# Optimization experiments

Hardware: AMD Instinct MI355X
Metric: run time of the kernel (lower is better)

## Reference

```python
import jax, jax.numpy as jnp
import numpy as np

B, T, D = 2, 2048, 2048
H, DH = 16, 128
FG = 5461
EPS = 1e-5
ROPE_BASE = 10000.0


def rmsnorm(x, w):
    rms = jax.lax.rsqrt(jnp.mean(x * x, axis=-1, keepdims=True) + EPS)
    return x * rms * w


def rotate_half(x):
    x1 = x[..., ::2]
    x2 = x[..., 1::2]
    return jnp.stack((-x2, x1), axis=-1).reshape(x.shape)


def rope_tables(t_len, dh, dtype):
    inv_freq = 1.0 / (ROPE_BASE ** (np.arange(0, dh, 2, dtype=np.float32) / dh))
    t = np.arange(t_len, dtype=np.float32)
    freqs = np.outer(t, inv_freq)                 # [T, dh/2]
    emb = np.repeat(freqs, 2, axis=-1)            # repeat_interleave -> [T, dh]
    return jnp.asarray(np.cos(emb), dtype), jnp.asarray(np.sin(emb), dtype)


def setup_inputs() -> dict:
    key = jax.random.key(0)
    ks = jax.random.split(key, 8)
    s_attn = 1.0 / np.sqrt(D)
    s_gate = 1.0 / np.sqrt(D)
    s_proj = 1.0 / np.sqrt(FG)
    return {
        "x": jax.random.normal(ks[0], (B, T, D), jnp.float32),
        "norm1_w": jnp.ones((D,), jnp.float32),
        "norm2_w": jnp.ones((D,), jnp.float32),
        "c_attn_w": jax.random.normal(ks[1], (3 * D, D), jnp.float32) * s_attn,
        "c_proj_w": jax.random.normal(ks[2], (D, D), jnp.float32) * s_attn,
        "c_gate_w": jax.random.normal(ks[3], (FG, D), jnp.float32) * s_gate,
        "c_val_w": jax.random.normal(ks[4], (FG, D), jnp.float32) * s_gate,
        "c_mlp_proj_w": jax.random.normal(ks[5], (D, FG), jnp.float32) * s_proj,
    }


def block(x, norm1_w, norm2_w, c_attn_w, c_proj_w, c_gate_w, c_val_w, c_mlp_proj_w):
    # ---- attention branch (pre-norm) ----
    h = rmsnorm(x, norm1_w)
    qkv = h @ c_attn_w.T                                   # [B,T,3D]
    qkv = qkv.reshape(B, T, 3, H, DH).transpose(2, 0, 3, 1, 4)
    q, k, v = qkv[0], qkv[1], qkv[2]                       # [B,H,T,DH]
    cos, sin = rope_tables(T, DH, x.dtype)                 # [T,DH]
    q = q * cos + rotate_half(q) * sin
    k = k * cos + rotate_half(k) * sin
    att = jnp.einsum("bhqd,bhkd->bhqk", q, k) * (1.0 / np.sqrt(DH))
    causal = jnp.tril(jnp.ones((T, T), bool))
    att = jnp.where(causal, att, -jnp.inf)
    att = jax.nn.softmax(att, axis=-1)
    y = jnp.einsum("bhqk,bhkd->bhqd", att, v)              # [B,H,T,DH]
    y = y.transpose(0, 2, 1, 3).reshape(B, T, D)
    x = x + y @ c_proj_w.T
    # ---- MLP branch (pre-norm, SwiGLU) ----
    h = rmsnorm(x, norm2_w)
    gate = jax.nn.silu(h @ c_gate_w.T)                     # [B,T,FG]
    val = h @ c_val_w.T
    x = x + (gate * val) @ c_mlp_proj_w.T
    return x


def reference(x, norm1_w, norm2_w, c_attn_w, c_proj_w, c_gate_w, c_val_w, c_mlp_proj_w):
    return block(x, norm1_w, norm2_w, c_attn_w, c_proj_w, c_gate_w, c_val_w, c_mlp_proj_w)
```

## Files before the change

### kernel.cpp

```cpp
#include <hip/hip_runtime.h>
#include <hip/hip_bf16.h>
#include <stdint.h>

typedef __bf16 bf16_t;
typedef __bf16 bf16x8 __attribute__((ext_vector_type(8)));
typedef float  f32x4  __attribute__((ext_vector_type(4)));

#define DEV __device__ __forceinline__

constexpr int   Bn = 2, Tn = 2048, Dn = 2048, Hn = 16, DHn = 128;
constexpr int   BTn = Bn * Tn;
constexpr int   TD3 = 3 * Dn;
constexpr int   FGn = 5461, FGPn = 5504;
constexpr float EPSf   = 1e-5f;
constexpr float LOG2E  = 1.4426950408889634f;
constexpr float ASCALE = 0.08838834764831845f;
constexpr float LN1E4  = 9.210340371976184f;

DEV void gld16(void* lds, const void* g) {
  __builtin_amdgcn_global_load_lds(
      (__attribute__((address_space(1))) void*)(void*)g,
      (__attribute__((address_space(3))) void*)lds, 16, 0, 0);
}

DEV bf16x8 dsr128(const bf16_t* p) {
  bf16x8 r;
  asm volatile("ds_read_b128 %0, %1"
               : "=v"(r)
               : "v"((const __attribute__((address_space(3))) bf16_t*)p));
  return r;
}

__global__ __launch_bounds__(256)
void rmsnorm_k(const float* __restrict__ x, const float* __restrict__ w,
               bf16_t* __restrict__ out) {
  const int row = blockIdx.x;
  const int tid = threadIdx.x;
  const float* xr = x + (size_t)row * Dn;
  float4 a = ((const float4*)xr)[tid * 2];
  float4 b = ((const float4*)xr)[tid * 2 + 1];
  float ss = a.x*a.x + a.y*a.y + a.z*a.z + a.w*a.w
           + b.x*b.x + b.y*b.y + b.z*b.z + b.w*b.w;
#pragma unroll
  for (int off = 32; off > 0; off >>= 1) ss += __shfl_xor(ss, off, 64);
  __shared__ float red[4];
  if ((tid & 63) == 0) red[tid >> 6] = ss;
  __syncthreads();
  float tot = red[0] + red[1] + red[2] + red[3];
  float rms = rsqrtf(tot * (1.0f / Dn) + EPSf);
  float4 wa = ((const float4*)w)[tid * 2];
  float4 wb = ((const float4*)w)[tid * 2 + 1];
  bf16x8 o;
  o[0] = (bf16_t)(a.x * rms * wa.x); o[1] = (bf16_t)(a.y * rms * wa.y);
  o[2] = (bf16_t)(a.z * rms * wa.z); o[3] = (bf16_t)(a.w * rms * wa.w);
  o[4] = (bf16_t)(b.x * rms * wb.x); o[5] = (bf16_t)(b.y * rms * wb.y);
  o[6] = (bf16_t)(b.z * rms * wb.z); o[7] = (bf16_t)(b.w * rms * wb.w);
  *(bf16x8*)&out[(size_t)row * Dn + tid * 8] = o;
}

__global__ __launch_bounds__(256)
void cvt_pad_k(const float* __restrict__ src, bf16_t* __restrict__ dst,
               int srcR, int srcC, int dstC, int n8) {
  int i = blockIdx.x * 256 + threadIdx.x;
  if (i >= n8) return;
  long base = (long)i * 8;
  int r = (int)(base / dstC);
  int c = (int)(base % dstC);
  bf16x8 o;
#pragma unroll
  for (int k = 0; k < 8; ++k) {
    int cc = c + k;
    float v = (r < srcR && cc < srcC) ? src[(size_t)r * srcC + cc] : 0.0f;
    o[k] = (bf16_t)v;
  }
  *(bf16x8*)&dst[base] = o;
}

__global__ __launch_bounds__(256)
void reduce_k(float* __restrict__ out, const bf16_t* __restrict__ P0,
              const bf16_t* __restrict__ P1) {
  int i = blockIdx.x * 256 + threadIdx.x;
  bf16x8 p0 = *(const bf16x8*)&P0[(size_t)i * 8];
  bf16x8 p1 = *(const bf16x8*)&P1[(size_t)i * 8];
  float4 o0 = ((const float4*)out)[i * 2];
  float4 o1 = ((const float4*)out)[i * 2 + 1];
  o0.x += (float)p0[0] + (float)p1[0];
  o0.y += (float)p0[1] + (float)p1[1];
  o0.z += (float)p0[2] + (float)p1[2];
  o0.w += (float)p0[3] + (float)p1[3];
  o1.x += (float)p0[4] + (float)p1[4];
  o1.y += (float)p0[5] + (float)p1[5];
  o1.z += (float)p0[6] + (float)p1[6];
  o1.w += (float)p0[7] + (float)p1[7];
  ((float4*)out)[i * 2]     = o0;
  ((float4*)out)[i * 2 + 1] = o1;
}

__global__ __launch_bounds__(256)
void reduce2e(float* __restrict__ out, const float* __restrict__ E,
              const bf16_t* __restrict__ P0, const bf16_t* __restrict__ P1) {
  int i = blockIdx.x * 256 + threadIdx.x;
  bf16x8 p0 = *(const bf16x8*)&P0[(size_t)i * 8];
  bf16x8 p1 = *(const bf16x8*)&P1[(size_t)i * 8];
  float4 e0 = ((const float4*)E)[i * 2];
  float4 e1 = ((const float4*)E)[i * 2 + 1];
  float4 o0, o1;
  o0.x = e0.x + (float)p0[0] + (float)p1[0];
  o0.y = e0.y + (float)p0[1] + (float)p1[1];
  o0.z = e0.z + (float)p0[2] + (float)p1[2];
  o0.w = e0.w + (float)p0[3] + (float)p1[3];
  o1.x = e1.x + (float)p0[4] + (float)p1[4];
  o1.y = e1.y + (float)p0[5] + (float)p1[5];
  o1.z = e1.z + (float)p0[6] + (float)p1[6];
  o1.w = e1.w + (float)p0[7] + (float)p1[7];
  ((float4*)out)[i * 2]     = o0;
  ((float4*)out)[i * 2 + 1] = o1;
}

__global__ __launch_bounds__(256)
void reduce2b(bf16_t* __restrict__ outb, const bf16_t* __restrict__ P0,
              const bf16_t* __restrict__ P1) {
  int i = blockIdx.x * 256 + threadIdx.x;
  bf16x8 p0 = *(const bf16x8*)&P0[(size_t)i * 8];
  bf16x8 p1 = *(const bf16x8*)&P1[(size_t)i * 8];
  bf16x8 o;
#pragma unroll
  for (int k = 0; k < 8; ++k) o[k] = (bf16_t)((float)p0[k] + (float)p1[k]);
  *(bf16x8*)&outb[(size_t)i * 8] = o;
}

__global__ __launch_bounds__(512, 2)
void gemm_sk(const bf16_t* __restrict__ A, const bf16_t* __restrict__ W,
             bf16_t* __restrict__ P0, bf16_t* __restrict__ P1,
             int ldk, int klen, int ldc, int nby) {
  __shared__ __align__(128) bf16_t As[2][256 * 64];
  __shared__ __align__(128) bf16_t Bs[2][256 * 64];
  const int tid = threadIdx.x;
  const int lane = tid & 63, w = tid >> 6;
  const int wm = w >> 2, wn = w & 3;
  const int g = lane >> 4, q = lane & 15;

  const int nwg = gridDim.x;
  const int cpx = nwg >> 3;
  const int nid = (blockIdx.x & 7) * cpx + (blockIdx.x >> 3);
  const int half = nwg >> 1;
  const int s   = nid / half;
  const int rem = nid % half;
  const int bx = rem / nby, by = rem % nby;
  const int row0 = by * 256, col0 = bx * 256;
  const int kofs = s * klen;
  bf16_t* P = s ? P1 : P0;

  f32x4 acc[8][4] = {};

  const bf16_t* Asrc[4];
  const bf16_t* Wsrc[4];
  int aoff[4];
#pragma unroll
  for (int i = 0; i < 4; ++i) {
    int ci = i * 512 + tid;
    int r  = ci >> 3;
    int cs = (ci & 7) ^ (r & 7);
    Asrc[i] = A + (size_t)(row0 + r) * ldk + kofs + cs * 8;
    Wsrc[i] = W + (size_t)(col0 + r) * ldk + kofs + cs * 8;
    aoff[i] = i * 8192 + w * 1024;
  }

  int offA[2][8], offB[2][4];
#pragma unroll
  for (int kk = 0; kk < 2; ++kk) {
#pragma unroll
    for (int m = 0; m < 8; ++m) {
      int r = wm * 128 + m * 16 + q;
      offA[kk][m] = r * 128 + (((kk * 4 + g) ^ (r & 7)) * 16);
    }
#pragma unroll
    for (int n = 0; n < 4; ++n) {
      int r = wn * 64 + n * 16 + q;
      offB[kk][n] = r * 128 + (((kk * 4 + g) ^ (r & 7)) * 16);
    }
  }

  const int NT = klen >> 6;
  auto stage = [&](int T, int h) {
    const int slot = T & 1;
    const size_t kk = (size_t)T * 64;
#pragma unroll
    for (int i = 0; i < 2; ++i) {
      int rd = h * 2 + i;
      gld16((char*)As[slot] + aoff[rd], Asrc[rd] + kk);
      gld16((char*)Bs[slot] + aoff[rd], Wsrc[rd] + kk);
    }
  };

  bf16x8 af[8], bfr[4];

  auto half_rd = [&](const char* as_, const char* bs_, int kk) {
#pragma unroll
    for (int m = 0; m < 8; ++m) af[m] = dsr128((const bf16_t*)(as_ + offA[kk][m]));
#pragma unroll
    for (int n = 0; n < 4; ++n) bfr[n] = dsr128((const bf16_t*)(bs_ + offB[kk][n]));
  };
  auto mfmas = [&]() {
    asm volatile("s_waitcnt lgkmcnt(0)" ::: "memory");
    __builtin_amdgcn_sched_barrier(0);
    __builtin_amdgcn_s_setprio(1);
#pragma unroll
    for (int m = 0; m < 8; ++m)
#pragma unroll
      for (int n = 0; n < 4; ++n)
        acc[m][n] = __builtin_amdgcn_mfma_f32_16x16x32_bf16(af[m], bfr[n], acc[m][n], 0, 0, 0);
    __builtin_amdgcn_s_setprio(0);
    __builtin_amdgcn_sched_barrier(0);
  };

  stage(0, 0); stage(0, 1);
  asm volatile("s_waitcnt vmcnt(0)" ::: "memory");
  asm volatile("s_barrier" ::: "memory");

  for (int T = 0; T < NT; ++T) {
    const char* as_ = (const char*)As[T & 1];
    const char* bs_ = (const char*)Bs[T & 1];
    const bool st = (T + 1 < NT);
    half_rd(as_, bs_, 0);
    if (st) stage(T + 1, 0);
    mfmas();
    half_rd(as_, bs_, 1);
    if (st) stage(T + 1, 1);
    mfmas();
    if (st) asm volatile("s_waitcnt vmcnt(0)" ::: "memory");
    asm volatile("s_barrier" ::: "memory");
  }

#pragma unroll
  for (int m = 0; m < 8; ++m)
#pragma unroll
    for (int n = 0; n < 4; ++n)
#pragma unroll
      for (int j = 0; j < 4; ++j) {
        int r = row0 + wm * 128 + m * 16 + g * 4 + j;
        int c = col0 + wn * 64 + n * 16 + q;
        P[(size_t)r * ldc + c] = (bf16_t)acc[m][n][j];
      }
}

__global__ __launch_bounds__(512, 2)
void gemmgv(const bf16_t* __restrict__ A, const bf16_t* __restrict__ Wg,
            const bf16_t* __restrict__ Wv, bf16_t* __restrict__ Out,
            int K, int ldc, int nby) {
  __shared__ __align__(128) bf16_t As[2][256 * 64];
  __shared__ __align__(128) bf16_t Gs[2][128 * 64];
  __shared__ __align__(128) bf16_t Vs[2][128 * 64];
  const int tid = threadIdx.x;
  const int lane = tid & 63, w = tid >> 6;
  const int wm = w >> 2, wn = w & 3;
  const int g = lane >> 4, q = lane & 15;

  const int nwg = gridDim.x;
  const int cpx = nwg >> 3;
  const int nid = (blockIdx.x & 7) * cpx + (blockIdx.x >> 3);
  const int bx = nid / nby, by = nid % nby;
  const int row0 = by * 256, col0 = bx * 128;

  f32x4 accg[8][2] = {}, accv[8][2] = {};

  const bf16_t* Asrc[4];
  int aoff[4];
#pragma unroll
  for (int i = 0; i < 4; ++i) {
    int ci = i * 512 + tid;
    int r  = ci >> 3;
    int cs = (ci & 7) ^ (r & 7);
    Asrc[i] = A + (size_t)(row0 + r) * K + cs * 8;
    aoff[i] = i * 8192 + w * 1024;
  }
  const bf16_t* Gsrc[2];
  const bf16_t* Vsrc[2];
  int boff[2];
#pragma unroll
  for (int i = 0; i < 2; ++i) {
    int ci = i * 512 + tid;
    int r  = ci >> 3;
    int cs = (ci & 7) ^ (r & 7);
    Gsrc[i] = Wg + (size_t)(col0 + r) * K + cs * 8;
    Vsrc[i] = Wv + (size_t)(col0 + r) * K + cs * 8;
    boff[i] = i * 8192 + w * 1024;
  }

  int offA[2][8], offB[2][2];
#pragma unroll
  for (int kk = 0; kk < 2; ++kk) {
#pragma unroll
    for (int m = 0; m < 8; ++m) {
      int r = wm * 128 + m * 16 + q;
      offA[kk][m] = r * 128 + (((kk * 4 + g) ^ (r & 7)) * 16);
    }
#pragma unroll
    for (int n = 0; n < 2; ++n) {
      int r = wn * 32 + n * 16 + q;
      offB[kk][n] = r * 128 + (((kk * 4 + g) ^ (r & 7)) * 16);
    }
  }

  const int NT = K >> 6;
  auto stage = [&](int T, int h) {
    const int slot = T & 1;
    const size_t kk = (size_t)T * 64;
#pragma unroll
    for (int i = 0; i < 2; ++i) {
      int rd = h * 2 + i;
      gld16((char*)As[slot] + aoff[rd], Asrc[rd] + kk);
    }
    gld16((char*)Gs[slot] + boff[h], Gsrc[h] + kk);
    gld16((char*)Vs[slot] + boff[h], Vsrc[h] + kk);
  };

  bf16x8 af[8], bg[2], bv[2];

  auto half_rd = [&](const char* as_, const char* gs_, const char* vs_, int kk) {
#pragma unroll
    for (int m = 0; m < 8; ++m) af[m] = dsr128((const bf16_t*)(as_ + offA[kk][m]));
#pragma unroll
    for (int n = 0; n < 2; ++n) {
      bg[n] = dsr128((const bf16_t*)(gs_ + offB[kk][n]));
      bv[n] = dsr128((const bf16_t*)(vs_ + offB[kk][n]));
    }
  };
  auto mfmas = [&]() {
    asm volatile("s_waitcnt lgkmcnt(0)" ::: "memory");
    __builtin_amdgcn_sched_barrier(0);
    __builtin_amdgcn_s_setprio(1);
#pragma unroll
    for (int m = 0; m < 8; ++m)
#pragma unroll
      for (int n = 0; n < 2; ++n) {
        accg[m][n] = __builtin_amdgcn_mfma_f32_16x16x32_bf16(af[m], bg[n], accg[m][n], 0, 0, 0);
        accv[m][n] = __builtin_amdgcn_mfma_f32_16x16x32_bf16(af[m], bv[n], accv[m][n], 0, 0, 0);
      }
    __builtin_amdgcn_s_setprio(0);
    __builtin_amdgcn_sched_barrier(0);
  };

  stage(0, 0); stage(0, 1);
  asm volatile("s_waitcnt vmcnt(0)" ::: "memory");
  asm volatile("s_barrier" ::: "memory");

  for (int T = 0; T < NT; ++T) {
    const char* as_ = (const char*)As[T & 1];
    const char* gs_ = (const char*)Gs[T & 1];
    const char* vs_ = (const char*)Vs[T & 1];
    const bool st = (T + 1 < NT);
    half_rd(as_, gs_, vs_, 0);
    if (st) stage(T + 1, 0);
    mfmas();
    half_rd(as_, gs_, vs_, 1);
    if (st) stage(T + 1, 1);
    mfmas();
    if (st) asm volatile("s_waitcnt vmcnt(0)" ::: "memory");
    asm volatile("s_barrier" ::: "memory");
  }

#pragma unroll
  for (int m = 0; m < 8; ++m) {
#pragma unroll
    for (int n = 0; n < 2; ++n) {
#pragma unroll
      for (int j = 0; j < 4; ++j) {
        int r = row0 + wm * 128 + m * 16 + g * 4 + j;
        int c = col0 + wn * 32 + n * 16 + q;
        float gt = accg[m][n][j];
        float sg = gt / (1.0f + __expf(-gt));
        Out[(size_t)r * ldc + c] = (bf16_t)(sg * accv[m][n][j]);
      }
    }
  }
}

__global__ __launch_bounds__(256)
void rope_k(const bf16_t* __restrict__ qkv, bf16_t* __restrict__ Qb,
            bf16_t* __restrict__ Kb, bf16_t* __restrict__ Vt) {
  const int t0 = blockIdx.x * 32;
  const int bh = blockIdx.y;
  const int b = bh >> 4, hh = bh & 15;
  __shared__ bf16_t Vl[32][132];

#pragma unroll
  for (int it = 0; it < 2; ++it) {
    int task = threadIdx.x + it * 256;
    int tt = task >> 4, ck = task & 15, d0 = ck * 8;
    int tg = t0 + tt;
    const bf16_t* srow = qkv + (size_t)(b * Tn + tg) * TD3 + hh * DHn + d0;
    bf16x8 qv = *(const bf16x8*)(srow);
    bf16x8 kv = *(const bf16x8*)(srow + Dn);
    bf16x8 vv = *(const bf16x8*)(srow + 2 * Dn);
    bf16x8 qo, ko;
#pragma unroll
    for (int p = 0; p < 4; ++p) {
      int jj = (d0 >> 1) + p;
      float fr = __expf(-((float)(2 * jj) / 128.0f) * LN1E4);
      float ang = (float)tg * fr;
      float cs = cosf(ang), sn = sinf(ang);
      float qe = (float)qv[2 * p], qod = (float)qv[2 * p + 1];
      float ke = (float)kv[2 * p], kod = (float)kv[2 * p + 1];
      qo[2 * p]     = (bf16_t)((qe * cs - qod * sn) * ASCALE);
      qo[2 * p + 1] = (bf16_t)((qod * cs + qe * sn) * ASCALE);
      ko[2 * p]     = (bf16_t)(ke * cs - kod * sn);
      ko[2 * p + 1] = (bf16_t)(kod * cs + ke * sn);
    }
    *(bf16x8*)&Qb[((size_t)bh * Tn + tg) * DHn + d0] = qo;
    *(bf16x8*)&Kb[((size_t)bh * Tn + tg) * DHn + d0] = ko;
    *(bf16x8*)&Vl[tt][d0] = vv;
  }
  __syncthreads();
#pragma unroll
  for (int it = 0; it < 2; ++it) {
    int task = threadIdx.x + it * 256;
    int dd = task >> 2, tc = (task & 3) * 8;
    bf16x8 ov;
#pragma unroll
    for (int i = 0; i < 8; ++i) ov[i] = Vl[tc + i][dd];
    *(bf16x8*)&Vt[((size_t)bh * DHn + dd) * Tn + t0 + tc] = ov;
  }
}

__global__ __launch_bounds__(256, 2)
void attn_k(const bf16_t* __restrict__ Qb, const bf16_t* __restrict__ Kb,
            const bf16_t* __restrict__ Vt, bf16_t* __restrict__ Y) {
  const int orig = blockIdx.x + 16 * blockIdx.y;
  const int nid  = (orig & 7) * 64 + (orig >> 3);
  const int pi = nid & 15;
  const int bh = nid >> 4;
  const int b = bh >> 4, hh = bh & 15;
  const int tid = threadIdx.x, lane = tid & 63, w = tid >> 6;
  const int g = lane >> 4, q = lane & 15;
  const int iA = pi, iB = 31 - pi;
  const int kmax = iB;

  __shared__ bf16_t Ks[2][64 * 128];
  __shared__ bf16_t Vs[2][128 * 64];
  __shared__ bf16_t Ps[4][16 * 72];

  bf16x8 aqA[4], aqB[4];
  {
    const bf16_t* QrA = Qb + ((size_t)bh * Tn + iA * 64 + w * 16 + q) * DHn;
    const bf16_t* QrB = Qb + ((size_t)bh * Tn + iB * 64 + w * 16 + q) * DHn;
#pragma unroll
    for (int s = 0; s < 4; ++s) {
      aqA[s] = *(const bf16x8*)(QrA + s * 32 + g * 8);
      aqB[s] = *(const bf16x8*)(QrB + s * 32 + g * 8);
    }
  }

  f32x4 oA[8] = {}, oB[8] = {};
  float mA[4], lA[4], mB[4], lB[4];
#pragma unroll
  for (int j = 0; j < 4; ++j) {
    mA[j] = -__builtin_inff(); lA[j] = 0.0f;
    mB[j] = -__builtin_inff(); lB[j] = 0.0f;
  }

  auto stage = [&](int buf, int kt) {
    const int k0 = kt * 64;
#pragma unroll
    for (int l = 0; l < 4; ++l) {
      int ci = (w * 4 + l) * 64 + lane;
      int kr = ci >> 4, kc = (ci & 15) ^ (kr & 7);
      gld16((char*)Ks[buf] + (w * 4 + l) * 1024,
            Kb + ((size_t)bh * Tn + k0 + kr) * DHn + kc * 8);
      int vr = ci >> 3, vc = (ci & 7) ^ (vr & 7);
      gld16((char*)Vs[buf] + (w * 4 + l) * 1024,
            Vt + ((size_t)bh * DHn + vr) * Tn + k0 + vc * 8);
    }
  };

  stage(0, 0);

  for (int kt = 0; kt <= kmax; ++kt) {
    __syncthreads();
    if (kt < kmax) stage((kt + 1) & 1, kt + 1);
    const bf16_t* ks = Ks[kt & 1];
    const bf16_t* vs = Vs[kt & 1];
    const bool actA = (kt <= iA);
    const int k0 = kt * 64;

    f32x4 saA[4] = {}, saB[4] = {};
    __builtin_amdgcn_s_setprio(1);
    if (actA) {
#pragma unroll
      for (int s = 0; s < 4; ++s) {
#pragma unroll
        for (int n = 0; n < 4; ++n) {
          bf16x8 bk = *(const bf16x8*)&ks[(n * 16 + q) * 128 + (((s * 4 + g) ^ (q & 7)) * 8)];
          saA[n] = __builtin_amdgcn_mfma_f32_16x16x32_bf16(aqA[s], bk, saA[n], 0, 0, 0);
          saB[n] = __builtin_amdgcn_mfma_f32_16x16x32_bf16(aqB[s], bk, saB[n], 0, 0, 0);
        }
      }
    } else {
#pragma unroll
      for (int s = 0; s < 4; ++s) {
#pragma unroll
        for (int n = 0; n < 4; ++n) {
          bf16x8 bk = *(const bf16x8*)&ks[(n * 16 + q) * 128 + (((s * 4 + g) ^ (q & 7)) * 8)];
          saB[n] = __builtin_amdgcn_mfma_f32_16x16x32_bf16(aqB[s], bk, saB[n], 0, 0, 0);
        }
      }
    }
    __builtin_amdgcn_s_setprio(0);

    bf16x8 paA[2], paB[2];
    auto softmax_p = [&](f32x4* sa, float* mst, float* lst, int itile,
                         bf16x8* pa, int qrow) {
      if (kt == itile) {
#pragma unroll
        for (int n = 0; n < 4; ++n)
#pragma unroll
          for (int j = 0; j < 4; ++j) {
            int kc = k0 + n * 16 + q;
            int qr = qrow + g * 4 + j;
            if (kc > qr) sa[n][j] = -1e30f;
          }
      }
      float mx[4];
#pragma unroll
      for (int j = 0; j < 4; ++j) {
        mx[j] = fmaxf(fmaxf(sa[0][j], sa[1][j]), fmaxf(sa[2][j], sa[3][j]));
#pragma unroll
        for (int off = 1; off < 16; off <<= 1)
          mx[j] = fmaxf(mx[j], __shfl_xor(mx[j], off, 16));
      }
      float ps[4][4], rsum[4];
#pragma unroll
      for (int j = 0; j < 4; ++j) rsum[j] = 0.0f;
      float mnew[4], corr[4];
#pragma unroll
      for (int j = 0; j < 4; ++j) {
        mnew[j] = fmaxf(mst[j], mx[j]);
        corr[j] = exp2f((mst[j] - mnew[j]) * LOG2E);
      }
#pragma unroll
      for (int n = 0; n < 4; ++n)
#pragma unroll
        for (int j = 0; j < 4; ++j) {
          ps[n][j] = exp2f((sa[n][j] - mnew[j]) * LOG2E);
          rsum[j] += ps[n][j];
        }
#pragma unroll
      for (int j = 0; j < 4; ++j) {
#pragma unroll
        for (int off = 1; off < 16; off <<= 1)
          rsum[j] += __shfl_xor(rsum[j], off, 16);
        lst[j] = lst[j] * corr[j] + rsum[j];
        mst[j] = mnew[j];
      }
#pragma unroll
      for (int n = 0; n < 4; ++n)
#pragma unroll
        for (int j = 0; j < 4; ++j)
          Ps[w][(g * 4 + j) * 72 + n * 16 + q] = (bf16_t)ps[n][j];
#pragma unroll
      for (int s2 = 0; s2 < 2; ++s2)
        pa[s2] = *(const bf16x8*)&Ps[w][q * 72 + s2 * 32 + g * 8];
      return corr;
    };

    float cA[4], cB[4];
    if (actA) {
      auto c = softmax_p(saA, mA, lA, iA, paA, iA * 64 + w * 16);
#pragma unroll
      for (int j = 0; j < 4; ++j) cA[j] = c[j];
#pragma unroll
      for (int n8 = 0; n8 < 8; ++n8)
#pragma unroll
        for (int j = 0; j < 4; ++j) oA[n8][j] *= cA[j];
    }
    {
      auto c = softmax_p(saB, mB, lB, iB, paB, iB * 64 + w * 16);
#pragma unroll
      for (int j = 0; j < 4; ++j) cB[j] = c[j];
#pragma unroll
      for (int n8 = 0; n8 < 8; ++n8)
#pragma unroll
        for (int j = 0; j < 4; ++j) oB[n8][j] *= cB[j];
    }

    __builtin_amdgcn_s_setprio(1);
    if (actA) {
#pragma unroll
      for (int s2 = 0; s2 < 2; ++s2)
#pragma unroll
        for (int n8 = 0; n8 < 8; ++n8) {
          bf16x8 bv = *(const bf16x8*)&vs[(n8 * 16 + q) * 64 + (((s2 * 4 + g) ^ (q & 7)) * 8)];
          oA[n8] = __builtin_amdgcn_mfma_f32_16x16x32_bf16(paA[s2], bv, oA[n8], 0, 0, 0);
          oB[n8] = __builtin_amdgcn_mfma_f32_16x16x32_bf16(paB[s2], bv, oB[n8], 0, 0, 0);
        }
    } else {
#pragma unroll
      for (int s2 = 0; s2 < 2; ++s2)
#pragma unroll
        for (int n8 = 0; n8 < 8; ++n8) {
          bf16x8 bv = *(const bf16x8*)&vs[(n8 * 16 + q) * 64 + (((s2 * 4 + g) ^ (q & 7)) * 8)];
          oB[n8] = __builtin_amdgcn_mfma_f32_16x16x32_bf16(paB[s2], bv, oB[n8], 0, 0, 0);
        }
    }
    __builtin_amdgcn_s_setprio(0);
  }

#pragma unroll
  for (int n8 = 0; n8 < 8; ++n8)
#pragma unroll
    for (int j = 0; j < 4; ++j) {
      int trA = iA * 64 + w * 16 + g * 4 + j;
      int trB = iB * 64 + w * 16 + g * 4 + j;
      Y[(size_t)(b * Tn + trA) * Dn + hh * DHn + n8 * 16 + q] =
          (bf16_t)(oA[n8][j] / lA[j]);
      Y[(size_t)(b * Tn + trB) * Dn + hh * DHn + n8 * 16 + q] =
          (bf16_t)(oB[n8][j] / lB[j]);
    }
}

extern "C" void kernel_launch(void* const* d_in, const int* in_sizes, int n_in,
                              void* d_out, int out_size, void* d_ws, size_t ws_size,
                              hipStream_t stream) {
  const float* x      = (const float*)d_in[0];
  const float* n1w    = (const float*)d_in[1];
  const float* n2w    = (const float*)d_in[2];
  const float* attn_w = (const float*)d_in[3];
  const float* proj_w = (const float*)d_in[4];
  const float* gate_w = (const float*)d_in[5];
  const float* val_w  = (const float*)d_in[6];
  const float* mlp_w  = (const float*)d_in[7];

  char* ws = (char*)d_ws;
  bf16_t* h    = (bf16_t*)(ws);
  bf16_t* bufA = (bf16_t*)(ws + 16777216);
  bf16_t* bufB = (bf16_t*)(ws + 67108864);
  bf16_t* wb   = (bf16_t*)(ws + 117440512);

  bf16_t* Pq0  = bufB;
  bf16_t* Pq1  = bufA;
  bf16_t* qkv  = bufA;
  bf16_t* Qb   = bufB;
  bf16_t* Kb   = Qb + (size_t)32 * Tn * DHn;
  bf16_t* Vt   = Kb + (size_t)32 * Tn * DHn;
  bf16_t* y    = h;
  bf16_t* Pp0  = bufA;
  bf16_t* Pp1  = bufA + (size_t)BTn * Dn;
  bf16_t* wbV  = bufA;
  bf16_t* gv   = bufB;
  bf16_t* Pm0  = h;
  bf16_t* Pm1  = bufA;
  float*  out  = (float*)d_out;

  rmsnorm_k<<<BTn, 256, 0, stream>>>(x, n1w, h);
  cvt_pad_k<<<(TD3 * Dn / 8 + 255) / 256, 256, 0, stream>>>(attn_w, wb, TD3, Dn, Dn, TD3 * Dn / 8);
  gemm_sk<<<768, 512, 0, stream>>>(h, wb, Pq0, Pq1, Dn, Dn / 2, TD3, BTn / 256);
  reduce2b<<<BTn * TD3 / 8 / 256, 256, 0, stream>>>(qkv, Pq0, Pq1);
  rope_k<<<dim3(Tn / 32, 32), 256, 0, stream>>>(qkv, Qb, Kb, Vt);
  attn_k<<<dim3(16, 32), 256, 0, stream>>>(Qb, Kb, Vt, y);
  cvt_pad_k<<<(Dn * Dn / 8 + 255) / 256, 256, 0, stream>>>(proj_w, wb, Dn, Dn, Dn, Dn * Dn / 8);
  gemm_sk<<<256, 512, 0, stream>>>(y, wb, Pp0, Pp1, Dn, Dn / 2, Dn, BTn / 256);
  reduce2e<<<BTn * Dn / 8 / 256, 256, 0, stream>>>(out, x, Pp0, Pp1);
  rmsnorm_k<<<BTn, 256, 0, stream>>>(out, n2w, h);
  cvt_pad_k<<<(FGPn * Dn / 8 + 255) / 256, 256, 0, stream>>>(gate_w, wb, FGn, Dn, Dn, FGPn * Dn / 8);
  cvt_pad_k<<<(FGPn * Dn / 8 + 255) / 256, 256, 0, stream>>>(val_w, wbV, FGn, Dn, Dn, FGPn * Dn / 8);
  gemmgv<<<(FGPn / 128) * (BTn / 256), 512, 0, stream>>>(h, wb, wbV, gv, Dn, FGPn, BTn / 256);
  cvt_pad_k<<<(Dn * FGPn / 8 + 255) / 256, 256, 0, stream>>>(mlp_w, wb, Dn, FGn, FGPn, Dn * FGPn / 8);
  gemm_sk<<<256, 512, 0, stream>>>(gv, wb, Pm0, Pm1, FGPn, FGPn / 2, Dn, BTn / 256);
  reduce_k<<<BTn * Dn / 8 / 256, 256, 0, stream>>>(out, Pm0, Pm1);
}
```

Baseline: 730.2 us.

## Fuse split-K reductions into RoPE and residual RMSNorm kernels

```diff
diff --git a/kernel.cpp b/kernel.cpp
--- a/kernel.cpp
+++ b/kernel.cpp
@@ -56,6 +56,50 @@
   o[4] = (bf16_t)(b.x * rms * wb.x); o[5] = (bf16_t)(b.y * rms * wb.y);
   o[6] = (bf16_t)(b.z * rms * wb.z); o[7] = (bf16_t)(b.w * rms * wb.w);
   *(bf16x8*)&out[(size_t)row * Dn + tid * 8] = o;
+}
+
+__global__ __launch_bounds__(256)
+void rms_fused(const float* __restrict__ x, const bf16_t* __restrict__ P0,
+               const bf16_t* __restrict__ P1, const float* __restrict__ w,
+               float* __restrict__ out, bf16_t* __restrict__ h) {
+  const int row = blockIdx.x;
+  const int tid = threadIdx.x;
+  const size_t base = (size_t)row * Dn + tid * 8;
+  float4 a = ((const float4*)(x + base))[0];
+  float4 b = ((const float4*)(x + base))[1];
+  bf16x8 p0 = *(const bf16x8*)&P0[base];
+  bf16x8 p1 = *(const bf16x8*)&P1[base];
+  float v[8];
+  v[0] = a.x + (float)p0[0] + (float)p1[0];
+  v[1] = a.y + (float)p0[1] + (float)p1[1];
+  v[2] = a.z + (float)p0[2] + (float)p1[2];
+  v[3] = a.w + (float)p0[3] + (float)p1[3];
+  v[4] = b.x + (float)p0[4] + (float)p1[4];
+  v[5] = b.y + (float)p0[5] + (float)p1[5];
+  v[6] = b.z + (float)p0[6] + (float)p1[6];
+  v[7] = b.w + (float)p0[7] + (float)p1[7];
+  float4 o0 = {v[0], v[1], v[2], v[3]};
+  float4 o1 = {v[4], v[5], v[6], v[7]};
+  ((float4*)(out + base))[0] = o0;
+  ((float4*)(out + base))[1] = o1;
+  float ss = 0.f;
+#pragma unroll
+  for (int k = 0; k < 8; ++k) ss += v[k] * v[k];
+#pragma unroll
+  for (int off = 32; off > 0; off >>= 1) ss += __shfl_xor(ss, off, 64);
+  __shared__ float red[4];
+  if ((tid & 63) == 0) red[tid >> 6] = ss;
+  __syncthreads();
+  float tot = red[0] + red[1] + red[2] + red[3];
+  float rms = rsqrtf(tot * (1.0f / Dn) + EPSf);
+  float4 wa = ((const float4*)w)[tid * 2];
+  float4 wb = ((const float4*)w)[tid * 2 + 1];
+  bf16x8 o;
+  o[0] = (bf16_t)(v[0] * rms * wa.x); o[1] = (bf16_t)(v[1] * rms * wa.y);
+  o[2] = (bf16_t)(v[2] * rms * wa.z); o[3] = (bf16_t)(v[3] * rms * wa.w);
+  o[4] = (bf16_t)(v[4] * rms * wb.x); o[5] = (bf16_t)(v[5] * rms * wb.y);
+  o[6] = (bf16_t)(v[6] * rms * wb.z); o[7] = (bf16_t)(v[7] * rms * wb.w);
+  *(bf16x8*)&h[base] = o;
 }
 
 __global__ __launch_bounds__(256)
@@ -96,39 +140,6 @@
   ((float4*)out)[i * 2 + 1] = o1;
 }
 
-__global__ __launch_bounds__(256)
-void reduce2e(float* __restrict__ out, const float* __restrict__ E,
-              const bf16_t* __restrict__ P0, const bf16_t* __restrict__ P1) {
-  int i = blockIdx.x * 256 + threadIdx.x;
-  bf16x8 p0 = *(const bf16x8*)&P0[(size_t)i * 8];
-  bf16x8 p1 = *(const bf16x8*)&P1[(size_t)i * 8];
-  float4 e0 = ((const float4*)E)[i * 2];
-  float4 e1 = ((const float4*)E)[i * 2 + 1];
-  float4 o0, o1;
-  o0.x = e0.x + (float)p0[0] + (float)p1[0];
-  o0.y = e0.y + (float)p0[1] + (float)p1[1];
-  o0.z = e0.z + (float)p0[2] + (float)p1[2];
-  o0.w = e0.w + (float)p0[3] + (float)p1[3];
-  o1.x = e1.x + (float)p0[4] + (float)p1[4];
-  o1.y = e1.y + (float)p0[5] + (float)p1[5];
-  o1.z = e1.z + (float)p0[6] + (float)p1[6];
-  o1.w = e1.w + (float)p0[7] + (float)p1[7];
-  ((float4*)out)[i * 2]     = o0;
-  ((float4*)out)[i * 2 + 1] = o1;
-}
-
-__global__ __launch_bounds__(256)
-void reduce2b(bf16_t* __restrict__ outb, const bf16_t* __restrict__ P0,
-              const bf16_t* __restrict__ P1) {
-  int i = blockIdx.x * 256 + threadIdx.x;
-  bf16x8 p0 = *(const bf16x8*)&P0[(size_t)i * 8];
-  bf16x8 p1 = *(const bf16x8*)&P1[(size_t)i * 8];
-  bf16x8 o;
-#pragma unroll
-  for (int k = 0; k < 8; ++k) o[k] = (bf16_t)((float)p0[k] + (float)p1[k]);
-  *(bf16x8*)&outb[(size_t)i * 8] = o;
-}
-
 __global__ __launch_bounds__(512, 2)
 void gemm_sk(const bf16_t* __restrict__ A, const bf16_t* __restrict__ W,
              bf16_t* __restrict__ P0, bf16_t* __restrict__ P1,
@@ -377,8 +388,9 @@
 }
 
 __global__ __launch_bounds__(256)
-void rope_k(const bf16_t* __restrict__ qkv, bf16_t* __restrict__ Qb,
-            bf16_t* __restrict__ Kb, bf16_t* __restrict__ Vt) {
+void rope_fused(const bf16_t* __restrict__ P0, const bf16_t* __restrict__ P1,
+                bf16_t* __restrict__ Qb, bf16_t* __restrict__ Kb,
+                bf16_t* __restrict__ Vt) {
   const int t0 = blockIdx.x * 32;
   const int bh = blockIdx.y;
   const int b = bh >> 4, hh = bh & 15;
@@ -389,27 +401,34 @@
     int task = threadIdx.x + it * 256;
     int tt = task >> 4, ck = task & 15, d0 = ck * 8;
     int tg = t0 + tt;
-    const bf16_t* srow = qkv + (size_t)(b * Tn + tg) * TD3 + hh * DHn + d0;
-    bf16x8 qv = *(const bf16x8*)(srow);
-    bf16x8 kv = *(const bf16x8*)(srow + Dn);
-    bf16x8 vv = *(const bf16x8*)(srow + 2 * Dn);
-    bf16x8 qo, ko;
+    const size_t rb = (size_t)(b * Tn + tg) * TD3 + hh * DHn + d0;
+    bf16x8 q0 = *(const bf16x8*)&P0[rb];
+    bf16x8 q1 = *(const bf16x8*)&P1[rb];
+    bf16x8 k0 = *(const bf16x8*)&P0[rb + Dn];
+    bf16x8 k1 = *(const bf16x8*)&P1[rb + Dn];
+    bf16x8 v0 = *(const bf16x8*)&P0[rb + 2 * Dn];
+    bf16x8 v1 = *(const bf16x8*)&P1[rb + 2 * Dn];
+    bf16x8 qo, ko, vo;
 #pragma unroll
     for (int p = 0; p < 4; ++p) {
       int jj = (d0 >> 1) + p;
       float fr = __expf(-((float)(2 * jj) / 128.0f) * LN1E4);
       float ang = (float)tg * fr;
       float cs = cosf(ang), sn = sinf(ang);
-      float qe = (float)qv[2 * p], qod = (float)qv[2 * p + 1];
-      float ke = (float)kv[2 * p], kod = (float)kv[2 * p + 1];
+      float qe = (float)q0[2 * p] + (float)q1[2 * p];
+      float qod = (float)q0[2 * p + 1] + (float)q1[2 * p + 1];
+      float ke = (float)k0[2 * p] + (float)k1[2 * p];
+      float kod = (float)k0[2 * p + 1] + (float)k1[2 * p + 1];
       qo[2 * p]     = (bf16_t)((qe * cs - qod * sn) * ASCALE);
       qo[2 * p + 1] = (bf16_t)((qod * cs + qe * sn) * ASCALE);
       ko[2 * p]     = (bf16_t)(ke * cs - kod * sn);
       ko[2 * p + 1] = (bf16_t)(kod * cs + ke * sn);
+      vo[2 * p]     = (bf16_t)((float)v0[2 * p] + (float)v1[2 * p]);
+      vo[2 * p + 1] = (bf16_t)((float)v0[2 * p + 1] + (float)v1[2 * p + 1]);
     }
     *(bf16x8*)&Qb[((size_t)bh * Tn + tg) * DHn + d0] = qo;
     *(bf16x8*)&Kb[((size_t)bh * Tn + tg) * DHn + d0] = ko;
-    *(bf16x8*)&Vl[tt][d0] = vv;
+    *(bf16x8*)&Vl[tt][d0] = vo;
   }
   __syncthreads();
 #pragma unroll
@@ -638,10 +657,9 @@
 
   bf16_t* Pq0  = bufB;
   bf16_t* Pq1  = bufA;
-  bf16_t* qkv  = bufA;
-  bf16_t* Qb   = bufB;
-  bf16_t* Kb   = Qb + (size_t)32 * Tn * DHn;
-  bf16_t* Vt   = Kb + (size_t)32 * Tn * DHn;
+  bf16_t* Qb   = wb;
+  bf16_t* Kb   = (bf16_t*)d_out;
+  bf16_t* Vt   = (bf16_t*)d_out + (size_t)32 * Tn * DHn;
   bf16_t* y    = h;
   bf16_t* Pp0  = bufA;
   bf16_t* Pp1  = bufA + (size_t)BTn * Dn;
@@ -654,13 +672,11 @@
   rmsnorm_k<<<BTn, 256, 0, stream>>>(x, n1w, h);
   cvt_pad_k<<<(TD3 * Dn / 8 + 255) / 256, 256, 0, stream>>>(attn_w, wb, TD3, Dn, Dn, TD3 * Dn / 8);
   gemm_sk<<<768, 512, 0, stream>>>(h, wb, Pq0, Pq1, Dn, Dn / 2, TD3, BTn / 256);
-  reduce2b<<<BTn * TD3 / 8 / 256, 256, 0, stream>>>(qkv, Pq0, Pq1);
-  rope_k<<<dim3(Tn / 32, 32), 256, 0, stream>>>(qkv, Qb, Kb, Vt);
+  rope_fused<<<dim3(Tn / 32, 32), 256, 0, stream>>>(Pq0, Pq1, Qb, Kb, Vt);
   attn_k<<<dim3(16, 32), 256, 0, stream>>>(Qb, Kb, Vt, y);
   cvt_pad_k<<<(Dn * Dn / 8 + 255) / 256, 256, 0, stream>>>(proj_w, wb, Dn, Dn, Dn, Dn * Dn / 8);
   gemm_sk<<<256, 512, 0, stream>>>(y, wb, Pp0, Pp1, Dn, Dn / 2, Dn, BTn / 256);
-  reduce2e<<<BTn * Dn / 8 / 256, 256, 0, stream>>>(out, x, Pp0, Pp1);
-  rmsnorm_k<<<BTn, 256, 0, stream>>>(out, n2w, h);
+  rms_fused<<<BTn, 256, 0, stream>>>(x, Pp0, Pp1, n2w, out, h);
   cvt_pad_k<<<(FGPn * Dn / 8 + 255) / 256, 256, 0, stream>>>(gate_w, wb, FGn, Dn, Dn, FGPn * Dn / 8);
   cvt_pad_k<<<(FGPn * Dn / 8 + 255) / 256, 256, 0, stream>>>(val_w, wbV, FGn, Dn, Dn, FGPn * Dn / 8);
   gemmgv<<<(FGPn / 128) * (BTn / 256), 512, 0, stream>>>(h, wb, wbV, gv, Dn, FGPn, BTn / 256);
```

After: 710.2 us, median of 2. -2.7%, faster.
